# Performance work log

Hardware: AMD Instinct MI355X
Metric: run time of the kernel (lower is better)

Reference implementation:

```python
import jax, jax.numpy as jnp
import numpy as np

GC = 128      # mem_dim
HEADS = 4     # gc / att_head_dim
HD = 32       # att_head_dim


def _dwconv(x, w, b, pad):
    # depthwise conv, NCHW, weight OIHW with I=1, groups=GC
    y = jax.lax.conv_general_dilated(
        x, w, window_strides=(1, 1),
        padding=((pad[0], pad[0]), (pad[1], pad[1])),
        feature_group_count=GC,
        dimension_numbers=('NCHW', 'OIHW', 'NCHW'))
    return y + b[None, :, None, None]


def setup_inputs() -> dict:
    key = jax.random.key(0)
    ks = jax.random.split(key, 5)
    x = jax.random.normal(ks[0], (32, 512, 56, 56), dtype=jnp.float32)
    w_dw1 = jax.random.normal(ks[1], (GC, 1, 3, 3), dtype=jnp.float32) * 0.1
    b_dw1 = jnp.zeros((GC,), jnp.float32)
    w_dw2 = jax.random.normal(ks[2], (GC, 1, 7, 7), dtype=jnp.float32) * 0.05
    b_dw2 = jnp.zeros((GC,), jnp.float32)
    w_qk = jax.random.normal(ks[3], (2 * GC, GC, 1, 1), dtype=jnp.float32) * (1.0 / np.sqrt(GC))
    b_qk = jnp.zeros((2 * GC,), jnp.float32)
    return {"x": x, "w_dw1": w_dw1, "b_dw1": b_dw1, "w_dw2": w_dw2,
            "b_dw2": b_dw2, "w_qk": w_qk, "b_qk": b_qk}


def reference(x, w_dw1, b_dw1, w_dw2, b_dw2, w_qk, b_qk):
    B, C, H, W = x.shape
    HW = H * W
    # grasp_memory + asymmetric_decouple (split along channels)
    m0 = C - 3 * GC
    mem = x[:, :m0]
    feat_att = x[:, m0:m0 + GC]
    feat_conv1 = x[:, m0 + GC:m0 + 2 * GC]
    feat_conv2 = x[:, m0 + 2 * GC:]
    feat_conv1 = _dwconv(feat_conv1, w_dw1, b_dw1, (1, 1))
    feat_conv2 = _dwconv(feat_conv2, w_dw2, b_dw2, (3, 3))
    # 1x1 conv qk -> [B, 2*GC, H, W]
    qk = jnp.einsum('bchw,oc->bohw', feat_att, w_qk[:, :, 0, 0]) + b_qk[None, :, None, None]
    qk = qk.reshape(B, 2 * GC, HW)
    q = qk[:, :GC].reshape(B, HEADS, HD, HW).transpose(0, 1, 3, 2)   # [B,h,HW,d]
    k = qk[:, GC:].reshape(B, HEADS, HD, HW).transpose(0, 1, 3, 2)
    v = feat_att.reshape(B, HEADS, HD, HW).transpose(0, 1, 3, 2)
    q = jax.nn.elu(q) + 1.0
    k = jax.nn.elu(k) + 1.0
    kmean = k.mean(axis=2, keepdims=True)                            # [B,h,1,d]
    z = 1.0 / (jnp.einsum('bhnd,bhmd->bhnm', q, kmean) + 1e-6)       # [B,h,HW,1]
    kv = jnp.einsum('bhnd,bhne->bhde', k, v) / HW                    # [B,h,d,d]
    att = jnp.einsum('bhnd,bhde->bhne', q, kv) * z                   # [B,h,HW,d]
    feat_att_out = att.transpose(0, 1, 3, 2).reshape(B, GC, H, W)
    feats = jnp.concatenate([feat_att_out, feat_conv1, feat_conv2], axis=1)
    return (mem, feats)
```

## Files before the change

### kernel.cpp

```cpp
#include <hip/hip_runtime.h>
#include <hip/hip_bf16.h>

#define Bn   32
#define Cn   512
#define GCn  128
#define HWn  3136
#define M0   128

#define Q_ELEMS  (Bn*GCn*HWn)
#define KV_ELEMS (Bn*4*32*32)
#define KS_ELEMS (Bn*4*32)

typedef __attribute__((ext_vector_type(8))) short bf16x8;
typedef __attribute__((ext_vector_type(4))) float f32x4;

__device__ __forceinline__ float bf2f(unsigned short u) {
    union { unsigned int i; float f; } v; v.i = ((unsigned int)u) << 16; return v.f;
}
__device__ __forceinline__ unsigned short f2bf(float f) {
    union { __hip_bfloat16 h; unsigned short u; } v; v.h = __float2bfloat16(f); return v.u;
}
__device__ __forceinline__ float act_elu1(float v) {
    return v > 0.0f ? v + 1.0f : __expf(v);
}

__global__ __launch_bounds__(256) void k_pre(
    const float* __restrict__ w_qk, unsigned short* __restrict__ wfrag,
    float* __restrict__ kvz) {
    const int t = threadIdx.x;
    if (blockIdx.x < 128) {
        int idx = blockIdx.x * 256 + t;
        int j  = idx & 7;
        int l  = (idx >> 3) & 63;
        int ks = (idx >> 9) & 3;
        int mt = idx >> 11;
        int o = mt * 16 + (l & 15);
        int c = ks * 32 + (l >> 4) * 8 + j;
        wfrag[idx] = f2bf(w_qk[o * 128 + c]);
    } else {
        int i = (blockIdx.x - 128) * 256 + t;
        kvz[i] = 0.0f;
    }
}

__global__ __launch_bounds__(256) void k_main(
    const float* __restrict__ x, const unsigned short* __restrict__ wfrag,
    const float* __restrict__ b_qk,
    unsigned short* __restrict__ q_ws, float* __restrict__ kv_g,
    float* __restrict__ ks_g) {

    __shared__ float Xl[128 * 66];
    __shared__ unsigned short Klds[128 * 72];

    const int t  = threadIdx.x;
    const int n0 = blockIdx.x * 64;
    const int b  = blockIdx.y;
    const float* xa = x + ((long long)(b * Cn + M0)) * HWn;

    #pragma unroll
    for (int p = 0; p < 8; ++p) {
        int idx4 = p * 256 + t;
        int c = idx4 >> 4, j4 = idx4 & 15;
        float4 v = *(const float4*)(xa + (long long)c * HWn + n0 + j4 * 4);
        float* d = Xl + c * 66 + j4 * 4;
        *(float2*)(d)     = make_float2(v.x, v.y);
        *(float2*)(d + 2) = make_float2(v.z, v.w);
    }
    __syncthreads();

    const int w = t >> 6, l = t & 63, nn = l & 15, q = l >> 4;
    f32x4 acc[4][4] = {};

    #pragma unroll
    for (int ks = 0; ks < 4; ++ks) {
        bf16x8 bq[4];
        #pragma unroll
        for (int in = 0; in < 4; ++in) {
            const float* src = Xl + (ks * 32 + q * 8) * 66 + in * 16 + nn;
            short tmp[8];
            #pragma unroll
            for (int j = 0; j < 8; ++j) tmp[j] = (short)f2bf(src[j * 66]);
            bq[in] = *(bf16x8*)tmp;
        }
        #pragma unroll
        for (int im = 0; im < 4; ++im) {
            const int mt = 4 * w + im;
            bf16x8 aq = *(const bf16x8*)(wfrag + ((mt * 4 + ks) * 64 + l) * 8);
            #pragma unroll
            for (int in = 0; in < 4; ++in)
                acc[im][in] = __builtin_amdgcn_mfma_f32_16x16x32_bf16(aq, bq[in], acc[im][in], 0, 0, 0);
        }
    }

    #pragma unroll
    for (int im = 0; im < 4; ++im) {
        const int obase = w * 64 + im * 16 + q * 4;
        float4 bias4 = *(const float4*)(b_qk + obase);
        if (w < 2) {
            #pragma unroll
            for (int r = 0; r < 4; ++r) {
                const float bias = ((const float*)&bias4)[r];
                unsigned short* dst = q_ws + ((long long)(b * GCn + obase + r)) * HWn + n0 + nn;
                #pragma unroll
                for (int in = 0; in < 4; ++in)
                    dst[in * 16] = f2bf(act_elu1(acc[im][in][r] + bias));
            }
        } else {
            const int krow = obase - 128;
            #pragma unroll
            for (int r = 0; r < 4; ++r) {
                const float bias = ((const float*)&bias4)[r];
                #pragma unroll
                for (int in = 0; in < 4; ++in)
                    Klds[(krow + r) * 72 + in * 16 + nn] = f2bf(act_elu1(acc[im][in][r] + bias));
            }
        }
    }
    __syncthreads();

    const int h = w;
    f32x4 akv[2][2] = {};
    float ksl0 = 0.0f, ksl1 = 0.0f;
    #pragma unroll
    for (int kt = 0; kt < 2; ++kt) {
        bf16x8 af0 = *(const bf16x8*)(Klds + (h * 32 + nn) * 72 + kt * 32 + q * 8);
        bf16x8 af1 = *(const bf16x8*)(Klds + (h * 32 + 16 + nn) * 72 + kt * 32 + q * 8);
        {
            const unsigned short* a0 = (const unsigned short*)&af0;
            const unsigned short* a1 = (const unsigned short*)&af1;
            #pragma unroll
            for (int j = 0; j < 8; ++j) { ksl0 += bf2f(a0[j]); ksl1 += bf2f(a1[j]); }
        }
        #pragma unroll
        for (int nt = 0; nt < 2; ++nt) {
            const float* vsrc = Xl + (h * 32 + nt * 16 + nn) * 66 + kt * 32 + q * 8;
            short tb[8];
            #pragma unroll
            for (int j = 0; j < 8; ++j) tb[j] = (short)f2bf(vsrc[j]);
            bf16x8 bv = *(bf16x8*)tb;
            akv[0][nt] = __builtin_amdgcn_mfma_f32_16x16x32_bf16(af0, bv, akv[0][nt], 0, 0, 0);
            akv[1][nt] = __builtin_amdgcn_mfma_f32_16x16x32_bf16(af1, bv, akv[1][nt], 0, 0, 0);
        }
    }
    const int bh = b * 4 + h;
    #pragma unroll
    for (int mt = 0; mt < 2; ++mt)
        #pragma unroll
        for (int nt = 0; nt < 2; ++nt)
            #pragma unroll
            for (int r = 0; r < 4; ++r)
                atomicAdd(&kv_g[(bh << 10) + (mt * 16 + q * 4 + r) * 32 + nt * 16 + nn],
                          akv[mt][nt][r]);
    float s0 = ksl0; s0 += __shfl_xor(s0, 16, 64); s0 += __shfl_xor(s0, 32, 64);
    float s1 = ksl1; s1 += __shfl_xor(s1, 16, 64); s1 += __shfl_xor(s1, 32, 64);
    if (l < 16) {
        atomicAdd(&ks_g[bh * 32 + nn],      s0);
        atomicAdd(&ks_g[bh * 32 + 16 + nn], s1);
    }
}

__device__ __forceinline__ void att_dev(
    const unsigned short* __restrict__ q_ws, const float* __restrict__ kv_g,
    const float* __restrict__ ks_g, float* __restrict__ feats,
    float* kvl, float* kml, int gx, int h, int b) {

    const int t = threadIdx.x;
    const int bh = b * 4 + h;
    const float inv = 1.0f / 3136.0f;
    #pragma unroll
    for (int p = 0; p < 4; ++p) kvl[t + p * 256] = kv_g[(bh << 10) + t + p * 256] * inv;
    if (t < 32) kml[t] = ks_g[bh * 32 + t] * inv;
    __syncthreads();

    const int n2 = gx * 256 + t;
    if (n2 >= 1568) return;
    const unsigned short* qp = q_ws + ((long long)(b * GCn + h * 32)) * HWn + n2 * 2;
    float a0[32], a1[32];
    float z0 = 1e-6f, z1 = 1e-6f;
    #pragma unroll
    for (int e = 0; e < 32; ++e) { a0[e] = 0.f; a1[e] = 0.f; }
    #pragma unroll 4
    for (int d = 0; d < 32; ++d) {
        const unsigned int qq = *(const unsigned int*)(qp + (long long)d * HWn);
        const float q0 = bf2f((unsigned short)qq);
        const float q1 = bf2f((unsigned short)(qq >> 16));
        z0 = __builtin_fmaf(q0, kml[d], z0);
        z1 = __builtin_fmaf(q1, kml[d], z1);
        #pragma unroll
        for (int e = 0; e < 32; ++e) {
            const float kv = kvl[d * 32 + e];
            a0[e] = __builtin_fmaf(q0, kv, a0[e]);
            a1[e] = __builtin_fmaf(q1, kv, a1[e]);
        }
    }
    z0 = 1.f / z0; z1 = 1.f / z1;
    float* op = feats + ((long long)(b * 384 + h * 32)) * HWn + n2 * 2;
    #pragma unroll
    for (int e = 0; e < 32; ++e)
        *(float2*)(op + (long long)e * HWn) = make_float2(a0[e] * z0, a1[e] * z1);
}

template<int KS, int PAD, int CIN, int COUT>
__device__ __forceinline__ void dwconv_dev(
    const float* __restrict__ x, const float* __restrict__ wg,
    const float* __restrict__ bg, float* __restrict__ feats, int c, int b) {

    const float* in = x + ((long long)(b * Cn + CIN + c)) * HWn;
    float* op = feats + ((long long)(b * 384 + COUT + c)) * HWn;

    float wr[KS * KS];
    #pragma unroll
    for (int i = 0; i < KS * KS; ++i) wr[i] = wg[c * KS * KS + i];
    const float bias = bg[c];

    for (int item = threadIdx.x; item < 784; item += 256) {
        const int y  = item / 14;
        const int xq = (item % 14) * 4;
        float acc[4] = {bias, bias, bias, bias};
        #pragma unroll
        for (int dy = 0; dy < KS; ++dy) {
            const int yy = y + dy - PAD;
            if (yy < 0 || yy >= 56) continue;
            const float* row = in + yy * 56 + xq;
            float r[12];
            float4 f;
            if (xq >= 4) f = *(const float4*)(row - 4); else f = make_float4(0, 0, 0, 0);
            r[0] = f.x; r[1] = f.y; r[2] = f.z; r[3] = f.w;
            f = *(const float4*)(row);
            r[4] = f.x; r[5] = f.y; r[6] = f.z; r[7] = f.w;
            if (xq <= 48) f = *(const float4*)(row + 4); else f = make_float4(0, 0, 0, 0);
            r[8] = f.x; r[9] = f.y; r[10] = f.z; r[11] = f.w;
            #pragma unroll
            for (int dx = 0; dx < KS; ++dx) {
                const float wv = wr[dy * KS + dx];
                #pragma unroll
                for (int j = 0; j < 4; ++j)
                    acc[j] = __builtin_fmaf(wv, r[j + dx + 4 - PAD], acc[j]);
            }
        }
        *(float4*)(op + y * 56 + xq) = make_float4(acc[0], acc[1], acc[2], acc[3]);
    }
}

__global__ __launch_bounds__(256) void k_post(
    const float* __restrict__ x,
    const unsigned short* __restrict__ q_ws, const float* __restrict__ kv_g,
    const float* __restrict__ ks_g,
    const float* __restrict__ w_dw1, const float* __restrict__ b_dw1,
    const float* __restrict__ w_dw2, const float* __restrict__ b_dw2,
    float* __restrict__ mem_out, float* __restrict__ feats) {

    __shared__ float kvl[1024];
    __shared__ float kml[32];
    const int bid = blockIdx.x;

    if (bid < 4096) {
        dwconv_dev<7, 3, 384, 256>(x, w_dw2, b_dw2, feats, bid & 127, bid >> 7);
    } else if (bid < 8192) {
        const int r = bid - 4096;
        dwconv_dev<3, 1, 256, 128>(x, w_dw1, b_dw1, feats, r & 127, r >> 7);
    } else if (bid < 9088) {
        const int r = bid - 8192;
        const int b = r / 28, rem = r % 28;
        att_dev(q_ws, kv_g, ks_g, feats, kvl, kml, rem % 7, rem / 7, b);
    } else {
        const int r = bid - 9088;
        for (int i4 = r * 256 + (int)threadIdx.x; i4 < 3211264; i4 += 2048 * 256) {
            int b  = i4 / 100352;
            int rr = i4 - b * 100352;
            ((float4*)mem_out)[i4] = ((const float4*)x)[(long long)b * 401408 + rr];
        }
    }
}

extern "C" void kernel_launch(void* const* d_in, const int* in_sizes, int n_in,
                              void* d_out, int out_size, void* d_ws, size_t ws_size,
                              hipStream_t stream) {
    const float* x     = (const float*)d_in[0];
    const float* w_dw1 = (const float*)d_in[1];
    const float* b_dw1 = (const float*)d_in[2];
    const float* w_dw2 = (const float*)d_in[3];
    const float* b_dw2 = (const float*)d_in[4];
    const float* w_qk  = (const float*)d_in[5];
    const float* b_qk  = (const float*)d_in[6];
    float* out = (float*)d_out;

    unsigned short* q_ws = (unsigned short*)d_ws;
    float* kv_g = (float*)(q_ws + (long long)Q_ELEMS);
    float* ks_g = kv_g + KV_ELEMS;
    unsigned short* wfrag = (unsigned short*)(ks_g + KS_ELEMS);

    float* mem_out = out;
    float* feats   = out + (long long)Bn * GCn * HWn;

    k_pre <<<656, 256, 0, stream>>>(w_qk, wfrag, kv_g);
    k_main<<<dim3(49, 32), 256, 0, stream>>>(x, wfrag, b_qk, q_ws, kv_g, ks_g);
    k_post<<<11136, 256, 0, stream>>>(x, q_ws, kv_g, ks_g,
                                      w_dw1, b_dw1, w_dw2, b_dw2, mem_out, feats);
}
```

Before: 489.0 us.

## Stage X as transposed bf16 in LDS, coalesce Q stores, tile dwconv via LDS

The QK GEMM kernel now converts the 128-channel X tile to bf16 once while loading it, stored n-major so MFMA B fragments become single vector LDS reads. Q results go to LDS and are written out with coalesced 16-byte stores instead of scattered 2-byte ones. V for the KV product is reread from global memory. The depthwise convs stage a zero-padded plane in shared memory and compute 8 outputs per thread, removing boundary branches and redundant global loads. The cost is extra syncs, transposed LDS writes that may hit bank conflicts, and the extra global V reads.

```diff
diff --git a/kernel.cpp b/kernel.cpp
--- a/kernel.cpp
+++ b/kernel.cpp
@@ -49,22 +49,27 @@
     unsigned short* __restrict__ q_ws, float* __restrict__ kv_g,
     float* __restrict__ ks_g) {
 
-    __shared__ float Xl[128 * 66];
+    __shared__ unsigned short Xn[64 * 144];
     __shared__ unsigned short Klds[128 * 72];
+    unsigned short* Qlds = Xn;
 
     const int t  = threadIdx.x;
     const int n0 = blockIdx.x * 64;
     const int b  = blockIdx.y;
     const float* xa = x + ((long long)(b * Cn + M0)) * HWn;
 
-    #pragma unroll
-    for (int p = 0; p < 8; ++p) {
-        int idx4 = p * 256 + t;
-        int c = idx4 >> 4, j4 = idx4 & 15;
-        float4 v = *(const float4*)(xa + (long long)c * HWn + n0 + j4 * 4);
-        float* d = Xl + c * 66 + j4 * 4;
-        *(float2*)(d)     = make_float2(v.x, v.y);
-        *(float2*)(d + 2) = make_float2(v.z, v.w);
+    {
+        const int c0 = t >> 1, half = t & 1;
+        const float* src = xa + (long long)c0 * HWn + n0 + half * 32;
+        #pragma unroll
+        for (int p = 0; p < 8; ++p) {
+            float4 v = *(const float4*)(src + p * 4);
+            const int n = half * 32 + p * 4;
+            Xn[(n + 0) * 144 + c0] = f2bf(v.x);
+            Xn[(n + 1) * 144 + c0] = f2bf(v.y);
+            Xn[(n + 2) * 144 + c0] = f2bf(v.z);
+            Xn[(n + 3) * 144 + c0] = f2bf(v.w);
+        }
     }
     __syncthreads();
 
@@ -75,13 +80,8 @@
     for (int ks = 0; ks < 4; ++ks) {
         bf16x8 bq[4];
         #pragma unroll
-        for (int in = 0; in < 4; ++in) {
-            const float* src = Xl + (ks * 32 + q * 8) * 66 + in * 16 + nn;
-            short tmp[8];
-            #pragma unroll
-            for (int j = 0; j < 8; ++j) tmp[j] = (short)f2bf(src[j * 66]);
-            bq[in] = *(bf16x8*)tmp;
-        }
+        for (int in = 0; in < 4; ++in)
+            bq[in] = *(const bf16x8*)(Xn + (in * 16 + nn) * 144 + ks * 32 + q * 8);
         #pragma unroll
         for (int im = 0; im < 4; ++im) {
             const int mt = 4 * w + im;
@@ -92,70 +92,92 @@
         }
     }
 
-    #pragma unroll
-    for (int im = 0; im < 4; ++im) {
-        const int obase = w * 64 + im * 16 + q * 4;
-        float4 bias4 = *(const float4*)(b_qk + obase);
-        if (w < 2) {
+    if (w >= 2) {
+        #pragma unroll
+        for (int im = 0; im < 4; ++im) {
+            const int obase = w * 64 + im * 16 + q * 4;
+            float4 bias4 = *(const float4*)(b_qk + obase);
+            const int krow = obase - 128;
             #pragma unroll
             for (int r = 0; r < 4; ++r) {
                 const float bias = ((const float*)&bias4)[r];
-                unsigned short* dst = q_ws + ((long long)(b * GCn + obase + r)) * HWn + n0 + nn;
                 #pragma unroll
                 for (int in = 0; in < 4; ++in)
-                    dst[in * 16] = f2bf(act_elu1(acc[im][in][r] + bias));
-            }
-        } else {
-            const int krow = obase - 128;
+                    Klds[(krow + r) * 72 + in * 16 + nn] = f2bf(act_elu1(acc[im][in][r] + bias));
+            }
+        }
+    }
+    __syncthreads();
+
+    if (w < 2) {
+        #pragma unroll
+        for (int im = 0; im < 4; ++im) {
+            const int obase = w * 64 + im * 16 + q * 4;
+            float4 bias4 = *(const float4*)(b_qk + obase);
             #pragma unroll
             for (int r = 0; r < 4; ++r) {
                 const float bias = ((const float*)&bias4)[r];
                 #pragma unroll
                 for (int in = 0; in < 4; ++in)
-                    Klds[(krow + r) * 72 + in * 16 + nn] = f2bf(act_elu1(acc[im][in][r] + bias));
-            }
-        }
-    }
-    __syncthreads();
-
-    const int h = w;
-    f32x4 akv[2][2] = {};
-    float ksl0 = 0.0f, ksl1 = 0.0f;
-    #pragma unroll
-    for (int kt = 0; kt < 2; ++kt) {
-        bf16x8 af0 = *(const bf16x8*)(Klds + (h * 32 + nn) * 72 + kt * 32 + q * 8);
-        bf16x8 af1 = *(const bf16x8*)(Klds + (h * 32 + 16 + nn) * 72 + kt * 32 + q * 8);
-        {
-            const unsigned short* a0 = (const unsigned short*)&af0;
-            const unsigned short* a1 = (const unsigned short*)&af1;
-            #pragma unroll
-            for (int j = 0; j < 8; ++j) { ksl0 += bf2f(a0[j]); ksl1 += bf2f(a1[j]); }
-        }
-        #pragma unroll
-        for (int nt = 0; nt < 2; ++nt) {
-            const float* vsrc = Xl + (h * 32 + nt * 16 + nn) * 66 + kt * 32 + q * 8;
-            short tb[8];
-            #pragma unroll
-            for (int j = 0; j < 8; ++j) tb[j] = (short)f2bf(vsrc[j]);
-            bf16x8 bv = *(bf16x8*)tb;
-            akv[0][nt] = __builtin_amdgcn_mfma_f32_16x16x32_bf16(af0, bv, akv[0][nt], 0, 0, 0);
-            akv[1][nt] = __builtin_amdgcn_mfma_f32_16x16x32_bf16(af1, bv, akv[1][nt], 0, 0, 0);
-        }
-    }
-    const int bh = b * 4 + h;
-    #pragma unroll
-    for (int mt = 0; mt < 2; ++mt)
-        #pragma unroll
-        for (int nt = 0; nt < 2; ++nt)
-            #pragma unroll
-            for (int r = 0; r < 4; ++r)
-                atomicAdd(&kv_g[(bh << 10) + (mt * 16 + q * 4 + r) * 32 + nt * 16 + nn],
-                          akv[mt][nt][r]);
-    float s0 = ksl0; s0 += __shfl_xor(s0, 16, 64); s0 += __shfl_xor(s0, 32, 64);
-    float s1 = ksl1; s1 += __shfl_xor(s1, 16, 64); s1 += __shfl_xor(s1, 32, 64);
-    if (l < 16) {
-        atomicAdd(&ks_g[bh * 32 + nn],      s0);
-        atomicAdd(&ks_g[bh * 32 + 16 + nn], s1);
+                    Qlds[(obase + r) * 72 + in * 16 + nn] = f2bf(act_elu1(acc[im][in][r] + bias));
+            }
+        }
+    }
+
+    {
+        const int h = w;
+        f32x4 akv[2][2] = {};
+        float ksl0 = 0.0f, ksl1 = 0.0f;
+        #pragma unroll
+        for (int kt = 0; kt < 2; ++kt) {
+            bf16x8 af0 = *(const bf16x8*)(Klds + (h * 32 + nn) * 72 + kt * 32 + q * 8);
+            bf16x8 af1 = *(const bf16x8*)(Klds + (h * 32 + 16 + nn) * 72 + kt * 32 + q * 8);
+            {
+                const unsigned short* a0 = (const unsigned short*)&af0;
+                const unsigned short* a1 = (const unsigned short*)&af1;
+                #pragma unroll
+                for (int j = 0; j < 8; ++j) { ksl0 += bf2f(a0[j]); ksl1 += bf2f(a1[j]); }
+            }
+            #pragma unroll
+            for (int nt = 0; nt < 2; ++nt) {
+                const float* vsrc = xa + (long long)(h * 32 + nt * 16 + nn) * HWn + n0 + kt * 32 + q * 8;
+                float4 v0 = *(const float4*)(vsrc);
+                float4 v1 = *(const float4*)(vsrc + 4);
+                short tb[8];
+                tb[0] = (short)f2bf(v0.x); tb[1] = (short)f2bf(v0.y);
+                tb[2] = (short)f2bf(v0.z); tb[3] = (short)f2bf(v0.w);
+                tb[4] = (short)f2bf(v1.x); tb[5] = (short)f2bf(v1.y);
+                tb[6] = (short)f2bf(v1.z); tb[7] = (short)f2bf(v1.w);
+                bf16x8 bv = *(bf16x8*)tb;
+                akv[0][nt] = __builtin_amdgcn_mfma_f32_16x16x32_bf16(af0, bv, akv[0][nt], 0, 0, 0);
+                akv[1][nt] = __builtin_amdgcn_mfma_f32_16x16x32_bf16(af1, bv, akv[1][nt], 0, 0, 0);
+            }
+        }
+        const int bh = b * 4 + h;
+        #pragma unroll
+        for (int mt = 0; mt < 2; ++mt)
+            #pragma unroll
+            for (int nt = 0; nt < 2; ++nt)
+                #pragma unroll
+                for (int r = 0; r < 4; ++r)
+                    atomicAdd(&kv_g[(bh << 10) + (mt * 16 + q * 4 + r) * 32 + nt * 16 + nn],
+                              akv[mt][nt][r]);
+        float s0 = ksl0; s0 += __shfl_xor(s0, 16, 64); s0 += __shfl_xor(s0, 32, 64);
+        float s1 = ksl1; s1 += __shfl_xor(s1, 16, 64); s1 += __shfl_xor(s1, 32, 64);
+        if (l < 16) {
+            atomicAdd(&ks_g[bh * 32 + nn],      s0);
+            atomicAdd(&ks_g[bh * 32 + 16 + nn], s1);
+        }
+    }
+    __syncthreads();
+
+    {
+        const int row = t >> 1, hf = t & 1;
+        const unsigned short* sp = Qlds + row * 72 + hf * 32;
+        unsigned short* dp = q_ws + ((long long)(b * GCn + row)) * HWn + n0 + hf * 32;
+        #pragma unroll
+        for (int p = 0; p < 4; ++p)
+            *(bf16x8*)(dp + p * 8) = *(const bf16x8*)(sp + p * 8);
     }
 }
 
@@ -203,42 +225,50 @@
 template<int KS, int PAD, int CIN, int COUT>
 __device__ __forceinline__ void dwconv_dev(
     const float* __restrict__ x, const float* __restrict__ wg,
-    const float* __restrict__ bg, float* __restrict__ feats, int c, int b) {
-
+    const float* __restrict__ bg, float* __restrict__ feats,
+    float* P, int c, int b) {
+
+    const int t = threadIdx.x;
     const float* in = x + ((long long)(b * Cn + CIN + c)) * HWn;
     float* op = feats + ((long long)(b * 384 + COUT + c)) * HWn;
 
+    constexpr int ROWS = 56 + 2 * PAD;
+    const float4 z4 = make_float4(0.f, 0.f, 0.f, 0.f);
+    for (int i = t; i < (ROWS * 68) >> 2; i += 256) ((float4*)P)[i] = z4;
+    __syncthreads();
+    for (int i = t; i < 784; i += 256) {
+        const int y = i / 14, xq = (i % 14) * 4;
+        *(float4*)(P + (y + PAD) * 68 + 4 + xq) = *(const float4*)(in + y * 56 + xq);
+    }
+    __syncthreads();
+
     float wr[KS * KS];
     #pragma unroll
     for (int i = 0; i < KS * KS; ++i) wr[i] = wg[c * KS * KS + i];
     const float bias = bg[c];
 
-    for (int item = threadIdx.x; item < 784; item += 256) {
-        const int y  = item / 14;
-        const int xq = (item % 14) * 4;
-        float acc[4] = {bias, bias, bias, bias};
+    for (int item = t; item < 392; item += 256) {
+        const int y  = item / 7;
+        const int xo = (item - y * 7) * 8;
+        float acc[8];
+        #pragma unroll
+        for (int j = 0; j < 8; ++j) acc[j] = bias;
         #pragma unroll
         for (int dy = 0; dy < KS; ++dy) {
-            const int yy = y + dy - PAD;
-            if (yy < 0 || yy >= 56) continue;
-            const float* row = in + yy * 56 + xq;
-            float r[12];
-            float4 f;
-            if (xq >= 4) f = *(const float4*)(row - 4); else f = make_float4(0, 0, 0, 0);
-            r[0] = f.x; r[1] = f.y; r[2] = f.z; r[3] = f.w;
-            f = *(const float4*)(row);
-            r[4] = f.x; r[5] = f.y; r[6] = f.z; r[7] = f.w;
-            if (xq <= 48) f = *(const float4*)(row + 4); else f = make_float4(0, 0, 0, 0);
-            r[8] = f.x; r[9] = f.y; r[10] = f.z; r[11] = f.w;
+            const float* rp = P + (y + dy) * 68 + xo;
+            float r[16];
+            #pragma unroll
+            for (int u = 0; u < 4; ++u) *(float4*)(r + 4 * u) = *(const float4*)(rp + 4 * u);
             #pragma unroll
             for (int dx = 0; dx < KS; ++dx) {
                 const float wv = wr[dy * KS + dx];
                 #pragma unroll
-                for (int j = 0; j < 4; ++j)
+                for (int j = 0; j < 8; ++j)
                     acc[j] = __builtin_fmaf(wv, r[j + dx + 4 - PAD], acc[j]);
             }
         }
-        *(float4*)(op + y * 56 + xq) = make_float4(acc[0], acc[1], acc[2], acc[3]);
+        *(float4*)(op + y * 56 + xo)     = make_float4(acc[0], acc[1], acc[2], acc[3]);
+        *(float4*)(op + y * 56 + xo + 4) = make_float4(acc[4], acc[5], acc[6], acc[7]);
     }
 }
 
@@ -250,19 +280,18 @@
     const float* __restrict__ w_dw2, const float* __restrict__ b_dw2,
     float* __restrict__ mem_out, float* __restrict__ feats) {
 
-    __shared__ float kvl[1024];
-    __shared__ float kml[32];
+    __shared__ float smem[62 * 68];
     const int bid = blockIdx.x;
 
     if (bid < 4096) {
-        dwconv_dev<7, 3, 384, 256>(x, w_dw2, b_dw2, feats, bid & 127, bid >> 7);
+        dwconv_dev<7, 3, 384, 256>(x, w_dw2, b_dw2, feats, smem, bid & 127, bid >> 7);
     } else if (bid < 8192) {
         const int r = bid - 4096;
-        dwconv_dev<3, 1, 256, 128>(x, w_dw1, b_dw1, feats, r & 127, r >> 7);
+        dwconv_dev<3, 1, 256, 128>(x, w_dw1, b_dw1, feats, smem, r & 127, r >> 7);
     } else if (bid < 9088) {
         const int r = bid - 8192;
         const int b = r / 28, rem = r % 28;
-        att_dev(q_ws, kv_g, ks_g, feats, kvl, kml, rem % 7, rem / 7, b);
+        att_dev(q_ws, kv_g, ks_g, feats, smem, smem + 1024, rem % 7, rem / 7, b);
     } else {
         const int r = bid - 9088;
         for (int i4 = r * 256 + (int)threadIdx.x; i4 < 3211264; i4 += 2048 * 256) {
```

Result: faster. 451.3 us (-7.7%).
